# Kernel tuning notes

Hardware: AMD Instinct MI355X
Metric: run time of the kernel (lower is better)

The kernel has to match this reference:

```python
import jax, jax.numpy as jnp
import numpy as np

N = 100_000   # active voxels
CIN = 64
COUT = 64
K = 3
L = 128       # voxel grid extent per axis
C = K // 2    # kernel center


def _offsets():
    # spatial offsets (z, y, x) for all non-center kernel taps, in the same
    # enumeration order as the original module's triple loop
    offs = []
    for dz in range(K):
        for dy in range(K):
            for dx in range(K):
                if (dz, dy, dx) != (C, C, C):
                    offs.append((dz - C, dy - C, dx - C))
    return offs


def _build_neighbor_map(coords):
    # coords: [N,3] int, unique. For each offset build (out_idx, in_idx) pairs
    # where voxel out_idx has an active neighbor in_idx at coords+offset.
    keys = (coords[:, 0].astype(np.int64) * L + coords[:, 1]) * L + coords[:, 2]
    order = np.argsort(keys)
    skeys = keys[order]
    pairs = []
    for (z, y, x) in _offsets():
        nb = coords + np.array([z, y, x], dtype=coords.dtype)
        valid = np.all((nb >= 0) & (nb < L), axis=1)
        nkeys = (nb[:, 0].astype(np.int64) * L + nb[:, 1]) * L + nb[:, 2]
        pos = np.clip(np.searchsorted(skeys, nkeys), 0, N - 1)
        found = valid & (skeys[pos] == nkeys)
        out_idx = np.nonzero(found)[0].astype(np.int32)
        in_idx = order[pos[found]].astype(np.int32)
        pairs.append((out_idx, in_idx))
    P = max(len(o) for o, _ in pairs)
    nei = np.zeros((len(pairs), P, 2), dtype=np.int32)
    sizes = np.zeros(len(pairs), dtype=np.int32)
    for i, (o, j) in enumerate(pairs):
        nei[i, :len(o), 0] = o
        nei[i, :len(o), 1] = j
        sizes[i] = len(o)
    return nei, sizes


def setup_inputs() -> dict:
    rng = np.random.default_rng(0)
    flat = rng.choice(L * L * L, size=N, replace=False)  # unique voxel coords
    coords = np.stack([flat // (L * L), (flat // L) % L, flat % L], axis=1).astype(np.int32)
    nei, sizes = _build_neighbor_map(coords)
    key = jax.random.key(0)
    k1, k2, k3 = jax.random.split(key, 3)
    sp_values = jax.random.normal(k1, (N, CIN), dtype=jnp.float32)
    weight = jax.random.normal(k2, (COUT, K, K, K, CIN), dtype=jnp.float32) * 0.05
    bias = jax.random.normal(k3, (COUT,), dtype=jnp.float32)
    return {"sp_values": sp_values, "weight": weight, "bias": bias,
            "nei_indices": jnp.asarray(nei), "nei_sizes": jnp.asarray(sizes)}


def reference(sp_values, weight, bias, nei_indices, nei_sizes):
    # weight: [Cout,kz,ky,kx,Cin] -> [kz,ky,kx,Cin,Cout] (matches torch permute)
    w = jnp.transpose(weight, (1, 2, 3, 4, 0))
    out = sp_values @ w[C, C, C]                                   # center tap: [N,Cout]
    offs = _offsets()
    w_offs = jnp.stack([w[z + C, y + C, x + C] for (z, y, x) in offs])  # [O,Cin,Cout]
    P = nei_indices.shape[1]
    valid = (jnp.arange(P)[None, :] < nei_sizes[:, None]).astype(sp_values.dtype)  # [O,P]
    gathered = sp_values[nei_indices[:, :, 1]] * valid[:, :, None]  # [O,P,Cin], padded rows zeroed
    contrib = jnp.einsum('opc,ocd->opd', gathered, w_offs)          # [O,P,Cout]
    out = out.at[nei_indices[:, :, 0].reshape(-1)].add(contrib.reshape(-1, out.shape[1]))
    return out + bias
```

## Files before the change

### kernel.cpp

```cpp
#include <hip/hip_runtime.h>


typedef __bf16 bf16x8 __attribute__((ext_vector_type(8)));
typedef float f32x4 __attribute__((ext_vector_type(4)));

#define LDSP 72

__device__ __forceinline__ unsigned short f2bf(float f) {
    union { float f; unsigned int u; } v; v.f = f;
    unsigned int u = v.u;
    return (unsigned short)((u + 0x7FFFu + ((u >> 16) & 1u)) >> 16);
}

__device__ __forceinline__ ushort4 cvt4(float4 v) {
    ushort4 b;
    b.x = f2bf(v.x); b.y = f2bf(v.y); b.z = f2bf(v.z); b.w = f2bf(v.w);
    return b;
}

__global__ __launch_bounds__(256) void sp3d_center(
    const float* __restrict__ sp, const float* __restrict__ w,
    const float* __restrict__ bias, float* __restrict__ out, int n_rows)
{
    __shared__ unsigned short Alds[64 * LDSP];
    __shared__ unsigned short Wlds[64 * LDSP];
    const int t = threadIdx.x;
    const int row0 = blockIdx.x * 64;

    for (int i = 0; i < 4; ++i) {
        int f4 = t + 256 * i;
        int n = f4 >> 4, k = (f4 & 15) << 2;
        float4 v = *(const float4*)&w[n * 1728 + 832 + k];
        *(ushort4*)&Wlds[n * LDSP + k] = cvt4(v);
    }
    {
        int r = t >> 2, q = t & 3;
        long rowg = row0 + r;
        if (rowg >= n_rows) rowg = n_rows - 1;
        for (int i = 0; i < 4; ++i) {
            int col = q * 4 + i * 16;
            float4 v = *(const float4*)&sp[rowg * 64 + col];
            *(ushort4*)&Alds[r * LDSP + col] = cvt4(v);
        }
    }
    __syncthreads();

    const int wid = t >> 6, lane = t & 63, ml = lane & 15, quad = lane >> 4;
    const bf16x8 a0 = *(const bf16x8*)&Alds[(wid * 16 + ml) * LDSP + quad * 8];
    const bf16x8 a1 = *(const bf16x8*)&Alds[(wid * 16 + ml) * LDSP + 32 + quad * 8];
    f32x4 acc[4];
    #pragma unroll
    for (int nt = 0; nt < 4; ++nt) {
        bf16x8 b0 = *(const bf16x8*)&Wlds[(nt * 16 + ml) * LDSP + quad * 8];
        bf16x8 b1 = *(const bf16x8*)&Wlds[(nt * 16 + ml) * LDSP + 32 + quad * 8];
        acc[nt] = f32x4{0.f, 0.f, 0.f, 0.f};
        acc[nt] = __builtin_amdgcn_mfma_f32_16x16x32_bf16(a0, b0, acc[nt], 0, 0, 0);
        acc[nt] = __builtin_amdgcn_mfma_f32_16x16x32_bf16(a1, b1, acc[nt], 0, 0, 0);
    }
    #pragma unroll
    for (int nt = 0; nt < 4; ++nt) {
        int col = nt * 16 + ml;
        float bv = bias[col];
        #pragma unroll
        for (int rg = 0; rg < 4; ++rg) {
            int row = row0 + wid * 16 + quad * 4 + rg;
            if (row < n_rows) out[row * 64 + col] = acc[nt][rg] + bv;
        }
    }
}

__global__ __launch_bounds__(256) void sp3d_scatter(
    const float* __restrict__ sp, const float* __restrict__ w,
    const int* __restrict__ nei, const int* __restrict__ sizes,
    float* __restrict__ out, int P)
{
    __shared__ unsigned short Alds[64 * LDSP];
    __shared__ unsigned short Wlds[64 * LDSP];
    __shared__ int sO[64];
    __shared__ int sI[64];

    const int o = blockIdx.y;
    const int size_o = sizes[o];
    const int chunk = blockIdx.x * 64;
    if (chunk >= size_o) return;
    const int t = threadIdx.x;
    const int tap = o + (o >= 13 ? 1 : 0);

    if (t < 64) {
        int p = chunk + t;
        if (p < size_o) {
            int2 pr = *(const int2*)&nei[(o * P + p) * 2];
            sO[t] = pr.x; sI[t] = pr.y;
        } else { sO[t] = -1; sI[t] = 0; }
    }
    for (int i = 0; i < 4; ++i) {
        int f4 = t + 256 * i;
        int n = f4 >> 4, k = (f4 & 15) << 2;
        float4 v = *(const float4*)&w[n * 1728 + tap * 64 + k];
        *(ushort4*)&Wlds[n * LDSP + k] = cvt4(v);
    }
    __syncthreads();

    {
        int r = t >> 2, q = t & 3;
        long rowg = sI[r];
        for (int i = 0; i < 4; ++i) {
            int col = q * 4 + i * 16;
            float4 v = *(const float4*)&sp[rowg * 64 + col];
            *(ushort4*)&Alds[r * LDSP + col] = cvt4(v);
        }
    }
    __syncthreads();

    const int wid = t >> 6, lane = t & 63, ml = lane & 15, quad = lane >> 4;
    const bf16x8 a0 = *(const bf16x8*)&Alds[(wid * 16 + ml) * LDSP + quad * 8];
    const bf16x8 a1 = *(const bf16x8*)&Alds[(wid * 16 + ml) * LDSP + 32 + quad * 8];
    f32x4 acc[4];
    #pragma unroll
    for (int nt = 0; nt < 4; ++nt) {
        bf16x8 b0 = *(const bf16x8*)&Wlds[(nt * 16 + ml) * LDSP + quad * 8];
        bf16x8 b1 = *(const bf16x8*)&Wlds[(nt * 16 + ml) * LDSP + 32 + quad * 8];
        acc[nt] = f32x4{0.f, 0.f, 0.f, 0.f};
        acc[nt] = __builtin_amdgcn_mfma_f32_16x16x32_bf16(a0, b0, acc[nt], 0, 0, 0);
        acc[nt] = __builtin_amdgcn_mfma_f32_16x16x32_bf16(a1, b1, acc[nt], 0, 0, 0);
    }
    #pragma unroll
    for (int nt = 0; nt < 4; ++nt) {
        int col = nt * 16 + ml;
        #pragma unroll
        for (int rg = 0; rg < 4; ++rg) {
            int rowl = wid * 16 + quad * 4 + rg;
            int go = sO[rowl];
            if (go >= 0) atomicAdd(&out[go * 64 + col], acc[nt][rg]);
        }
    }
}

extern "C" void kernel_launch(void* const* d_in, const int* in_sizes, int n_in,
                              void* d_out, int out_size, void* d_ws, size_t ws_size,
                              hipStream_t stream) {
    const float* sp    = (const float*)d_in[0];
    const float* w     = (const float*)d_in[1];
    const float* bias  = (const float*)d_in[2];
    const int*   nei   = (const int*)d_in[3];
    const int*   sizes = (const int*)d_in[4];
    float* out = (float*)d_out;

    const int N = in_sizes[0] / 64;
    const int P = in_sizes[3] / (26 * 2);

    dim3 g1((N + 63) / 64);
    sp3d_center<<<g1, 256, 0, stream>>>(sp, w, bias, out, N);

    dim3 g2((P + 63) / 64, 26);
    sp3d_scatter<<<g2, 256, 0, stream>>>(sp, w, nei, sizes, out, P);
}
```

Before: 115.9 us.

## Replace atomic scatter with output-stationary gather over dense neighbor table

```diff
diff --git a/kernel.cpp b/kernel.cpp
--- a/kernel.cpp
+++ b/kernel.cpp
@@ -18,120 +18,152 @@
     return b;
 }
 
-__global__ __launch_bounds__(256) void sp3d_center(
+__global__ __launch_bounds__(256) void sp3d_prep(
     const float* __restrict__ sp, const float* __restrict__ w,
-    const float* __restrict__ bias, float* __restrict__ out, int n_rows)
+    unsigned short* __restrict__ spb, unsigned short* __restrict__ wb,
+    int* __restrict__ tbl, int n_rows)
 {
-    __shared__ unsigned short Alds[64 * LDSP];
-    __shared__ unsigned short Wlds[64 * LDSP];
-    const int t = threadIdx.x;
-    const int row0 = blockIdx.x * 64;
+    const long gt = (long)blockIdx.x * 256 + threadIdx.x;
+    const long stride = (long)gridDim.x * 256;
 
-    for (int i = 0; i < 4; ++i) {
-        int f4 = t + 256 * i;
-        int n = f4 >> 4, k = (f4 & 15) << 2;
-        float4 v = *(const float4*)&w[n * 1728 + 832 + k];
-        *(ushort4*)&Wlds[n * LDSP + k] = cvt4(v);
+    const long ntbl = 26L * n_rows;
+    for (long i = gt; i < (ntbl >> 2); i += stride)
+        *(int4*)&tbl[i * 4] = make_int4(-1, -1, -1, -1);
+    if (gt < (ntbl & 3)) tbl[(ntbl & ~3L) + gt] = -1;
+
+    const long nsp = (long)n_rows * 16;
+    for (long i = gt; i < nsp; i += stride) {
+        float4 v = *(const float4*)&sp[i * 4];
+        *(ushort4*)&spb[i * 4] = cvt4(v);
     }
-    {
-        int r = t >> 2, q = t & 3;
-        long rowg = row0 + r;
-        if (rowg >= n_rows) rowg = n_rows - 1;
-        for (int i = 0; i < 4; ++i) {
-            int col = q * 4 + i * 16;
-            float4 v = *(const float4*)&sp[rowg * 64 + col];
-            *(ushort4*)&Alds[r * LDSP + col] = cvt4(v);
-        }
-    }
-    __syncthreads();
 
-    const int wid = t >> 6, lane = t & 63, ml = lane & 15, quad = lane >> 4;
-    const bf16x8 a0 = *(const bf16x8*)&Alds[(wid * 16 + ml) * LDSP + quad * 8];
-    const bf16x8 a1 = *(const bf16x8*)&Alds[(wid * 16 + ml) * LDSP + 32 + quad * 8];
-    f32x4 acc[4];
-    #pragma unroll
-    for (int nt = 0; nt < 4; ++nt) {
-        bf16x8 b0 = *(const bf16x8*)&Wlds[(nt * 16 + ml) * LDSP + quad * 8];
-        bf16x8 b1 = *(const bf16x8*)&Wlds[(nt * 16 + ml) * LDSP + 32 + quad * 8];
-        acc[nt] = f32x4{0.f, 0.f, 0.f, 0.f};
-        acc[nt] = __builtin_amdgcn_mfma_f32_16x16x32_bf16(a0, b0, acc[nt], 0, 0, 0);
-        acc[nt] = __builtin_amdgcn_mfma_f32_16x16x32_bf16(a1, b1, acc[nt], 0, 0, 0);
-    }
-    #pragma unroll
-    for (int nt = 0; nt < 4; ++nt) {
-        int col = nt * 16 + ml;
-        float bv = bias[col];
-        #pragma unroll
-        for (int rg = 0; rg < 4; ++rg) {
-            int row = row0 + wid * 16 + quad * 4 + rg;
-            if (row < n_rows) out[row * 64 + col] = acc[nt][rg] + bv;
-        }
+    for (long i = gt; i < 27 * 1024; i += stride) {
+        int tp = (int)(i >> 10);
+        int r  = (int)(i & 1023);
+        int n = r >> 4, k4 = r & 15;
+        float4 v = *(const float4*)&w[n * 1728 + tp * 64 + k4 * 4];
+        *(ushort4*)&wb[(tp * 64 + n) * 64 + k4 * 4] = cvt4(v);
     }
 }
 
-__global__ __launch_bounds__(256) void sp3d_scatter(
-    const float* __restrict__ sp, const float* __restrict__ w,
+__global__ __launch_bounds__(256) void sp3d_build(
     const int* __restrict__ nei, const int* __restrict__ sizes,
-    float* __restrict__ out, int P)
+    int* __restrict__ tbl, int n_rows, int P)
 {
-    __shared__ unsigned short Alds[64 * LDSP];
-    __shared__ unsigned short Wlds[64 * LDSP];
-    __shared__ int sO[64];
-    __shared__ int sI[64];
+    const int o = blockIdx.y;
+    const int p = blockIdx.x * 256 + threadIdx.x;
+    if (p < sizes[o]) {
+        int2 pr = *(const int2*)&nei[(o * P + p) * 2];
+        tbl[(long)o * n_rows + pr.x] = pr.y;
+    }
+}
 
-    const int o = blockIdx.y;
-    const int size_o = sizes[o];
-    const int chunk = blockIdx.x * 64;
-    if (chunk >= size_o) return;
+__global__ __launch_bounds__(256) void sp3d_main(
+    const unsigned short* __restrict__ spb, const unsigned short* __restrict__ wb,
+    const float* __restrict__ bias, const int* __restrict__ tbl,
+    float* __restrict__ out, int n_rows)
+{
+    __shared__ unsigned short Bt[2][64 * LDSP];
+    __shared__ int tl[26][256];
+
     const int t = threadIdx.x;
-    const int tap = o + (o >= 13 ? 1 : 0);
+    const int row0 = blockIdx.x * 256;
+    const int wid = t >> 6, lane = t & 63, ml = lane & 15, quad = lane >> 4;
 
-    if (t < 64) {
-        int p = chunk + t;
-        if (p < size_o) {
-            int2 pr = *(const int2*)&nei[(o * P + p) * 2];
-            sO[t] = pr.x; sI[t] = pr.y;
-        } else { sO[t] = -1; sI[t] = 0; }
+    {
+        int r = row0 + t;
+        if (r >= n_rows) r = n_rows - 1;
+        #pragma unroll
+        for (int o = 0; o < 26; ++o)
+            tl[o][t] = tbl[(long)o * n_rows + r];
     }
-    for (int i = 0; i < 4; ++i) {
-        int f4 = t + 256 * i;
-        int n = f4 >> 4, k = (f4 & 15) << 2;
-        float4 v = *(const float4*)&w[n * 1728 + tap * 64 + k];
-        *(ushort4*)&Wlds[n * LDSP + k] = cvt4(v);
+    {
+        int c = t;
+        *(bf16x8*)&Bt[0][(c >> 3) * LDSP + (c & 7) * 8] = *(const bf16x8*)(wb + c * 8);
+        c = t + 256;
+        *(bf16x8*)&Bt[0][(c >> 3) * LDSP + (c & 7) * 8] = *(const bf16x8*)(wb + c * 8);
     }
+
+    f32x4 acc[4][4];
+    #pragma unroll
+    for (int mg = 0; mg < 4; ++mg)
+        #pragma unroll
+        for (int nt = 0; nt < 4; ++nt) acc[mg][nt] = f32x4{0.f, 0.f, 0.f, 0.f};
+
     __syncthreads();
 
-    {
-        int r = t >> 2, q = t & 3;
-        long rowg = sI[r];
-        for (int i = 0; i < 4; ++i) {
-            int col = q * 4 + i * 16;
-            float4 v = *(const float4*)&sp[rowg * 64 + col];
-            *(ushort4*)&Alds[r * LDSP + col] = cvt4(v);
+    int cur = 0;
+    for (int tp = 0; tp < 27; ++tp) {
+        bf16x8 b0[4], b1[4];
+        #pragma unroll
+        for (int nt = 0; nt < 4; ++nt) {
+            b0[nt] = *(const bf16x8*)&Bt[cur][(nt * 16 + ml) * LDSP + quad * 8];
+            b1[nt] = *(const bf16x8*)&Bt[cur][(nt * 16 + ml) * LDSP + 32 + quad * 8];
         }
+
+        bf16x8 s0, s1;
+        if (tp < 26) {
+            const unsigned short* src = wb + (tp + 1) * 4096;
+            s0 = *(const bf16x8*)(src + t * 8);
+            s1 = *(const bf16x8*)(src + (t + 256) * 8);
+        }
+
+        int inr[4];
+        #pragma unroll
+        for (int mg = 0; mg < 4; ++mg) {
+            int rl = wid * 64 + mg * 16 + ml;
+            if (tp == 13) {
+                int r = row0 + rl;
+                inr[mg] = (r < n_rows) ? r : n_rows - 1;
+            } else {
+                int o = tp - (tp > 13 ? 1 : 0);
+                inr[mg] = tl[o][rl];
+            }
+        }
+
+        #pragma unroll
+        for (int mg = 0; mg < 4; ++mg) {
+            if (__any(inr[mg] >= 0)) {
+                bf16x8 a0, a1;
+                #pragma unroll
+                for (int j = 0; j < 8; ++j) { a0[j] = (__bf16)0.f; a1[j] = (__bf16)0.f; }
+                if (inr[mg] >= 0) {
+                    const unsigned short* ap = spb + (long)inr[mg] * 64 + quad * 8;
+                    a0 = *(const bf16x8*)ap;
+                    a1 = *(const bf16x8*)(ap + 32);
+                }
+                #pragma unroll
+                for (int nt = 0; nt < 4; ++nt) {
+                    acc[mg][nt] = __builtin_amdgcn_mfma_f32_16x16x32_bf16(a0, b0[nt], acc[mg][nt], 0, 0, 0);
+                    acc[mg][nt] = __builtin_amdgcn_mfma_f32_16x16x32_bf16(a1, b1[nt], acc[mg][nt], 0, 0, 0);
+                }
+            }
+        }
+
+        if (tp < 26) {
+            int c = t;
+            *(bf16x8*)&Bt[cur ^ 1][(c >> 3) * LDSP + (c & 7) * 8] = s0;
+            c = t + 256;
+            *(bf16x8*)&Bt[cur ^ 1][(c >> 3) * LDSP + (c & 7) * 8] = s1;
+        }
+        __syncthreads();
+        cur ^= 1;
     }
-    __syncthreads();
 
-    const int wid = t >> 6, lane = t & 63, ml = lane & 15, quad = lane >> 4;
-    const bf16x8 a0 = *(const bf16x8*)&Alds[(wid * 16 + ml) * LDSP + quad * 8];
-    const bf16x8 a1 = *(const bf16x8*)&Alds[(wid * 16 + ml) * LDSP + 32 + quad * 8];
-    f32x4 acc[4];
+    float bv[4];
     #pragma unroll
-    for (int nt = 0; nt < 4; ++nt) {
-        bf16x8 b0 = *(const bf16x8*)&Wlds[(nt * 16 + ml) * LDSP + quad * 8];
-        bf16x8 b1 = *(const bf16x8*)&Wlds[(nt * 16 + ml) * LDSP + 32 + quad * 8];
-        acc[nt] = f32x4{0.f, 0.f, 0.f, 0.f};
-        acc[nt] = __builtin_amdgcn_mfma_f32_16x16x32_bf16(a0, b0, acc[nt], 0, 0, 0);
-        acc[nt] = __builtin_amdgcn_mfma_f32_16x16x32_bf16(a1, b1, acc[nt], 0, 0, 0);
-    }
+    for (int nt = 0; nt < 4; ++nt) bv[nt] = bias[nt * 16 + ml];
     #pragma unroll
-    for (int nt = 0; nt < 4; ++nt) {
-        int col = nt * 16 + ml;
+    for (int mg = 0; mg < 4; ++mg) {
+        int rb = row0 + wid * 64 + mg * 16 + quad * 4;
         #pragma unroll
-        for (int rg = 0; rg < 4; ++rg) {
-            int rowl = wid * 16 + quad * 4 + rg;
-            int go = sO[rowl];
-            if (go >= 0) atomicAdd(&out[go * 64 + col], acc[nt][rg]);
+        for (int nt = 0; nt < 4; ++nt) {
+            int col = nt * 16 + ml;
+            #pragma unroll
+            for (int rg = 0; rg < 4; ++rg) {
+                int row = rb + rg;
+                if (row < n_rows) out[(long)row * 64 + col] = acc[mg][nt][rg] + bv[nt];
+            }
         }
     }
 }
@@ -149,9 +181,14 @@
     const int N = in_sizes[0] / 64;
     const int P = in_sizes[3] / (26 * 2);
 
-    dim3 g1((N + 63) / 64);
-    sp3d_center<<<g1, 256, 0, stream>>>(sp, w, bias, out, N);
+    char* ws = (char*)d_ws;
+    unsigned short* spb = (unsigned short*)ws;
+    size_t off = ((size_t)N * 64 * 2 + 255) & ~(size_t)255;
+    unsigned short* wb = (unsigned short*)(ws + off);
+    off = (off + 27 * 64 * 64 * 2 + 255) & ~(size_t)255;
+    int* tbl = (int*)(ws + off);
 
-    dim3 g2((P + 63) / 64, 26);
-    sp3d_scatter<<<g2, 256, 0, stream>>>(sp, w, nei, sizes, out, P);
+    sp3d_prep<<<dim3(1024), 256, 0, stream>>>(sp, w, spb, wb, tbl, N);
+    sp3d_build<<<dim3((P + 255) / 256, 26), 256, 0, stream>>>(nei, sizes, tbl, N, P);
+    sp3d_main<<<dim3((N + 255) / 256), 256, 0, stream>>>(spb, wb, bias, tbl, out, N);
 }
```

Measured after the change: 140.3 us. +21.1%, slower.
